# Performance work log

Measured on AMD Instinct MI355X. Metric: run time of the kernel, lower is better.

Reference implementation:

```python
import jax, jax.numpy as jnp
import numpy as np

S, B, I, H, L = 512, 64, 128, 256, 6  # seq_len, batch, input, hidden, layers


def setup_inputs() -> dict:
    key = jax.random.key(0)
    ks = jax.random.split(key, 8)
    sc = 1.0 / np.sqrt(H)
    return {
        "x": jax.random.normal(ks[0], (S, B, I), jnp.float32),
        "h0": jax.random.normal(ks[1], (2 * L, B, H), jnp.float32),
        "w_ih0": jax.random.normal(ks[2], (2, 3 * H, I), jnp.float32) * sc,
        "b_ih0": jax.random.normal(ks[3], (2, 3 * H), jnp.float32) * sc,
        "w_ih": jax.random.normal(ks[4], (L - 1, 2, 3 * H, 2 * H), jnp.float32) * sc,
        "b_ih": jax.random.normal(ks[5], (L - 1, 2, 3 * H), jnp.float32) * sc,
        "w_hh": jax.random.normal(ks[6], (L, 2, 3 * H, H), jnp.float32) * sc,
        "b_hh": jax.random.normal(ks[7], (L, 2, 3 * H), jnp.float32) * sc,
    }


def _gru_direction(gi_seq, h0d, whh, bhh, reverse):
    # gi_seq: (S, B, 3H) precomputed input gates; h0d: (B, H)
    if reverse:
        gi_seq = gi_seq[::-1]

    def step(h, gi):
        gh = h @ whh.T + bhh                       # (B, 3H)
        gi_r, gi_z, gi_n = jnp.split(gi, 3, axis=-1)
        gh_r, gh_z, gh_n = jnp.split(gh, 3, axis=-1)
        r = jax.nn.sigmoid(gi_r + gh_r)
        z = jax.nn.sigmoid(gi_z + gh_z)
        n = jnp.tanh(gi_n + r * gh_n)
        h_new = (1.0 - z) * n + z * h
        return h_new, h_new

    h_n, outs = jax.lax.scan(step, h0d, gi_seq)
    if reverse:
        outs = outs[::-1]
    return h_n, outs  # (B,H), (S,B,H)


def reference(x, h0, w_ih0, b_ih0, w_ih, b_ih, w_hh, b_hh):
    cur = x
    finals = []
    for l in range(L):
        wi = w_ih0 if l == 0 else w_ih[l - 1]
        bi = b_ih0 if l == 0 else b_ih[l - 1]
        # precompute input-gate projections for the whole sequence (big GEMM)
        gi_f = jnp.einsum('sbi,gi->sbg', cur, wi[0]) + bi[0]
        gi_b = jnp.einsum('sbi,gi->sbg', cur, wi[1]) + bi[1]
        h_f, out_f = _gru_direction(gi_f, h0[2 * l], w_hh[l, 0], b_hh[l, 0], False)
        h_b, out_b = _gru_direction(gi_b, h0[2 * l + 1], w_hh[l, 1], b_hh[l, 1], True)
        finals.append(h_f)
        finals.append(h_b)
        if l < L - 1:
            cur = jnp.concatenate([out_f, out_b], axis=-1)  # (S, B, 2H)
    return jnp.stack(finals)  # (2L, B, H)
```

## Files before the change

### kernel.cpp

```cpp
#include <hip/hip_runtime.h>
#include <hip/hip_bf16.h>
#include <cstddef>

#define S_LEN 512
#define BATCH 64
#define HID 256
#define G3 768
#define SB (S_LEN*BATCH)
#define D2 512
#define L2E 1.44269504f

typedef unsigned short u16;
typedef _Float16 h2v __attribute__((ext_vector_type(2)));
typedef __attribute__((ext_vector_type(8))) short s16x8;
typedef __attribute__((ext_vector_type(4))) float f32x4;

__device__ __forceinline__ float bf2f(u16 u) {
    return __uint_as_float(((unsigned)u) << 16);
}
__device__ __forceinline__ u16 f2bf(float f) {
    unsigned u = __float_as_uint(f);
    unsigned r = (u + 0x7FFFu + ((u >> 16) & 1u)) >> 16;
    return (u16)r;
}
__device__ __forceinline__ u16 f2h_bits(float f) {
    _Float16 h = (_Float16)f;
    union { _Float16 h; u16 u; } cv; cv.h = h;
    return cv.u;
}
__device__ __forceinline__ h2v u2h(unsigned u) {
    union { unsigned u; h2v h; } cv; cv.u = u;
    return cv.h;
}
__device__ __forceinline__ float dot2f(unsigned w, unsigned h, float acc) {
#if __has_builtin(__builtin_amdgcn_fdot2)
    return __builtin_amdgcn_fdot2(u2h(w), u2h(h), acc, false);
#else
    h2v wv = u2h(w), hv = u2h(h);
    return acc + (float)wv.x * (float)hv.x + (float)wv.y * (float)hv.y;
#endif
}
__device__ __forceinline__ float fast_rcp(float x) {
#if __has_builtin(__builtin_amdgcn_rcpf)
    return __builtin_amdgcn_rcpf(x);
#else
    return 1.f / x;
#endif
}
__device__ __forceinline__ float fast_exp2(float x) {
#if __has_builtin(__builtin_amdgcn_exp2f)
    return __builtin_amdgcn_exp2f(x);
#else
    return __expf(x * 0.69314718f);
#endif
}
__device__ __forceinline__ void gload_lds16(const void* g, void* l) {
    __builtin_amdgcn_global_load_lds((const __attribute__((address_space(1))) void*)g,
                                     (__attribute__((address_space(3))) void*)l, 16, 0, 0);
}

__global__ void f32_to_bf16(const float* __restrict__ in, u16* __restrict__ out, long n) {
    long i = (long)blockIdx.x * 256 + threadIdx.x;
    if (i < n) out[i] = f2bf(in[i]);
}
__global__ void f32_to_bf16_gs(const float* __restrict__ in, u16* __restrict__ out,
                               long n, int K) {
    long i = (long)blockIdx.x * 256 + threadIdx.x;
    if (i >= n) return;
    int g = (int)((i / K) % 768);
    float sc = (g < 512) ? L2E : (2.f * L2E);
    out[i] = f2bf(in[i] * sc);
}
__global__ void pack_whh_f16_gs(const float* __restrict__ in, unsigned* __restrict__ out,
                                long total) {
    long i = (long)blockIdx.x * 256 + threadIdx.x;
    if (i >= total) return;
    long mat = i / (128L * G3);
    long rem = i - mat * (128L * G3);
    int k2 = (int)(rem / G3);
    int g  = (int)(rem - (long)k2 * G3);
    float sc = (g < 512) ? L2E : (2.f * L2E);
    const float* base = in + mat * (768L * 256) + (long)g * 256 + 2 * k2;
    unsigned lo = f2h_bits(base[0] * sc);
    unsigned hi = f2h_bits(base[1] * sc);
    out[i] = lo | (hi << 16);
}
__global__ void add_bias(const float* __restrict__ bih0, const float* __restrict__ bihl,
                         const float* __restrict__ bhh, float* __restrict__ outb) {
    int i = blockIdx.x * 256 + threadIdx.x;
    if (i >= 6 * 1536) return;
    int l = i / 1536, r = i - l * 1536;
    int g = r % 768;
    float bi = (l == 0) ? bih0[r] : bihl[(l - 1) * 1536 + r];
    outb[i] = (g < 512) ? (bi + bhh[i]) * L2E : bi * (2.f * L2E);
}

__global__ __launch_bounds__(256, 2) void gemm_mfma(
    const u16* __restrict__ A,
    const u16* __restrict__ Bt,
    const float* __restrict__ bias,
    u16* __restrict__ Cg,
    int K)
{
    int d = blockIdx.z;
    const u16* Bb = Bt + (size_t)d * 768 * K;
    const float* bi = bias + d * G3;
    u16* Cm = Cg + (size_t)d * SB * G3;

    int n0 = blockIdx.x * 128;
    int m0 = blockIdx.y * 128;
    int tid = threadIdx.x;
    int wave = tid >> 6, lane = tid & 63;
    int wm = wave >> 1, wn = wave & 1;

    __shared__ u16 Asm[128 * 32];
    __shared__ u16 Bsm[128 * 32];

    f32x4 acc[4][4] = {};

    for (int k0 = 0; k0 < K; k0 += 32) {
#pragma unroll
        for (int p = 0; p < 2; p++) {
            int c = p * 256 + wave * 64 + lane;
            int row = c >> 2, kc = c & 3;
            const u16* srcA = A + (size_t)(m0 + row) * K + k0 + kc * 8;
            const u16* srcB = Bb + (size_t)(n0 + row) * K + k0 + kc * 8;
            gload_lds16(srcA, &Asm[(p * 256 + wave * 64) * 8]);
            gload_lds16(srcB, &Bsm[(p * 256 + wave * 64) * 8]);
        }
        __syncthreads();

        s16x8 af[4], bfr[4];
#pragma unroll
        for (int i = 0; i < 4; i++) {
            int arow = wm * 64 + i * 16 + (lane & 15);
            af[i] = *reinterpret_cast<const s16x8*>(&Asm[arow * 32 + (lane >> 4) * 8]);
            int brow = wn * 64 + i * 16 + (lane & 15);
            bfr[i] = *reinterpret_cast<const s16x8*>(&Bsm[brow * 32 + (lane >> 4) * 8]);
        }
#pragma unroll
        for (int i = 0; i < 4; i++)
#pragma unroll
            for (int j = 0; j < 4; j++)
                acc[i][j] = __builtin_amdgcn_mfma_f32_16x16x32_bf16(af[i], bfr[j], acc[i][j], 0, 0, 0);
        __syncthreads();
    }

    int lcol = lane & 15, lrow4 = (lane >> 4) * 4;
#pragma unroll
    for (int i = 0; i < 4; i++) {
#pragma unroll
        for (int j = 0; j < 4; j++) {
            int n = n0 + wn * 64 + j * 16 + lcol;
            float bv = bi[n];
#pragma unroll
            for (int q = 0; q < 4; q++) {
                int m = m0 + wm * 64 + i * 16 + lrow4 + q;
                Cm[(size_t)m * G3 + n] = f2bf(acc[i][j][q] + bv);
            }
        }
    }
}

__global__ __launch_bounds__(768, 3) void gru_scan(
    const unsigned* __restrict__ wpack,
    const float* __restrict__ bhh,
    const u16* __restrict__ gi,
    const float* __restrict__ h0,
    u16* __restrict__ outc,
    float* __restrict__ finals,
    int layer)
{
    int b = blockIdx.x;
    int d = blockIdx.y;
    int tid = threadIdx.x;

    int ld = layer * 2 + d;
    const unsigned* Wp = wpack + (size_t)ld * 128 * G3 + tid;
    const u16* gid = gi + (size_t)d * SB * G3;

    __shared__ float rz_s[512];
    __shared__ alignas(16) _Float16 h16_s[HID];
    __shared__ u16 gi_s[2][G3];

    unsigned wpk[128];
#pragma unroll
    for (int k = 0; k < 128; k++) wpk[k] = Wp[(size_t)k * G3];

    int gate = tid >> 8;
    int j = tid & 255;

    float hreg = 0.f, bhn = 0.f;
    if (gate == 2) {
        hreg = h0[(size_t)ld * BATCH * HID + b * HID + j];
        bhn = bhh[(size_t)ld * G3 + 512 + j] * (2.f * L2E);
        h16_s[j] = (_Float16)hreg;
    }
    {
        int s0 = d ? (S_LEN - 1) : 0;
        gi_s[0][tid] = gid[((size_t)s0 * BATCH + b) * G3 + tid];
    }
    __syncthreads();

    for (int t = 0; t < S_LEN; t++) {
        int s = d ? (S_LEN - 1 - t) : t;
        u16 ginext = 0;
        if (t + 1 < S_LEN) {
            int sn = d ? (s - 1) : (s + 1);
            ginext = gid[((size_t)sn * BATCH + b) * G3 + tid];
        }
        float acc = 0.f;
        const uint4* hp = reinterpret_cast<const uint4*>(h16_s);
#pragma unroll
        for (int k = 0; k < 32; k++) {
            uint4 q = hp[k];
            acc = dot2f(wpk[4 * k + 0], q.x, acc);
            acc = dot2f(wpk[4 * k + 1], q.y, acc);
            acc = dot2f(wpk[4 * k + 2], q.z, acc);
            acc = dot2f(wpk[4 * k + 3], q.w, acc);
        }
        float giv = bf2f(gi_s[t & 1][tid]);
        gi_s[(t + 1) & 1][tid] = ginext;
        if (gate < 2)
            rz_s[tid] = fast_rcp(1.f + fast_exp2(-(giv + acc)));
        __syncthreads();
        if (gate == 2) {
            float r = rz_s[j];
            float z = rz_s[256 + j];
            float xn2 = giv + r * (acc + bhn);
            float n = 1.f - 2.f * fast_rcp(fast_exp2(xn2) + 1.f);
            float hn = n + z * (hreg - n);
            hreg = hn;
            h16_s[j] = (_Float16)hn;
            outc[((size_t)s * BATCH + b) * D2 + d * HID + j] = f2bf(hn);
        }
        __syncthreads();
    }
    if (gate == 2)
        finals[(size_t)ld * BATCH * HID + b * HID + j] = hreg;
}

extern "C" void kernel_launch(void* const* d_in, const int* in_sizes, int n_in,
                              void* d_out, int out_size, void* d_ws, size_t ws_size,
                              hipStream_t stream) {
    const float* x     = (const float*)d_in[0];
    const float* h0    = (const float*)d_in[1];
    const float* w_ih0 = (const float*)d_in[2];
    const float* b_ih0 = (const float*)d_in[3];
    const float* w_ih  = (const float*)d_in[4];
    const float* b_ih  = (const float*)d_in[5];
    const float* w_hh  = (const float*)d_in[6];
    const float* b_hh  = (const float*)d_in[7];
    float* out = (float*)d_out;

    char* ws = (char*)d_ws;
    unsigned* wpack = (unsigned*)(ws + 0);
    u16* wbf0  = (u16*)(ws + 4718592);
    u16* wbfl  = (u16*)(ws + 5111808);
    float* biasT = (float*)(ws + 12976128);
    u16* gi    = (u16*)(ws + 13012992);
    u16* curA  = (u16*)(ws + 113676288);
    u16* curB  = (u16*)(ws + 147230720);

    pack_whh_f16_gs<<<(1179648 + 255) / 256, 256, 0, stream>>>(w_hh, wpack, 1179648L);
    f32_to_bf16_gs<<<(196608 + 255) / 256, 256, 0, stream>>>(w_ih0, wbf0, 196608L, 128);
    f32_to_bf16_gs<<<(3932160 + 255) / 256, 256, 0, stream>>>(w_ih, wbfl, 3932160L, 512);
    f32_to_bf16<<<(4194304 + 255) / 256, 256, 0, stream>>>(x, curA, 4194304L);
    add_bias<<<(9216 + 255) / 256, 256, 0, stream>>>(b_ih0, b_ih, b_hh, biasT);

    u16* cin = curA;
    u16* cout_ = curB;
    for (int l = 0; l < 6; l++) {
        int K = l ? 512 : 128;
        const u16* wt = l ? (wbfl + (size_t)(l - 1) * 2 * 768 * 512) : wbf0;
        const float* bi = biasT + (size_t)l * 1536;
        dim3 g(6, 256, 2);
        gemm_mfma<<<g, 256, 0, stream>>>(cin, wt, bi, gi, K);
        gru_scan<<<dim3(64, 2), 768, 0, stream>>>(wpack, b_hh, gi, h0,
                                                  cout_, out, l);
        u16* tmp = cin; cin = cout_; cout_ = tmp;
    }
}
```

Before: 3.913 ms.

## Split hidden dot across lane pairs to halve LDS reads in GRU scan

Repacks W_hh so each adjacent lane pair splits the k dimension: each lane reads only half of the hidden state from LDS and computes partial sums for both gates of the pair, then exchanges one partial with its neighbour via a shuffle. It also uses four independent accumulators to break the serial dot2 dependency chain. This aims to cut LDS bandwidth and latency in the recurrent step, at the cost of a cross-lane shuffle and a more complex weight layout.

```diff
diff --git a/kernel.cpp b/kernel.cpp
--- a/kernel.cpp
+++ b/kernel.cpp
@@ -71,16 +71,20 @@
     float sc = (g < 512) ? L2E : (2.f * L2E);
     out[i] = f2bf(in[i] * sc);
 }
-__global__ void pack_whh_f16_gs(const float* __restrict__ in, unsigned* __restrict__ out,
-                                long total) {
+__global__ void pack_whh_pair(const float* __restrict__ in, unsigned* __restrict__ out,
+                              long total) {
     long i = (long)blockIdx.x * 256 + threadIdx.x;
     if (i >= total) return;
     long mat = i / (128L * G3);
     long rem = i - mat * (128L * G3);
-    int k2 = (int)(rem / G3);
-    int g  = (int)(rem - (long)k2 * G3);
-    float sc = (g < 512) ? L2E : (2.f * L2E);
-    const float* base = in + mat * (768L * 256) + (long)g * 256 + 2 * k2;
+    int j = (int)(rem / G3);
+    int lane = (int)(rem - (long)j * G3);
+    int p = lane & 1;
+    int g0 = lane & ~1;
+    int gate = (j < 64) ? g0 : (g0 + 1);
+    int kp = 64 * p + ((j < 64) ? j : (j - 64));
+    float sc = (gate < 512) ? L2E : (2.f * L2E);
+    const float* base = in + mat * (768L * 256) + (long)gate * 256 + 2 * kp;
     unsigned lo = f2h_bits(base[0] * sc);
     unsigned hi = f2h_bits(base[1] * sc);
     out[i] = lo | (hi << 16);
@@ -163,7 +167,7 @@
 }
 
 __global__ __launch_bounds__(768, 3) void gru_scan(
-    const unsigned* __restrict__ wpack,
+    const unsigned* __restrict__ wpack2,
     const float* __restrict__ bhh,
     const u16* __restrict__ gi,
     const float* __restrict__ h0,
@@ -176,7 +180,7 @@
     int tid = threadIdx.x;
 
     int ld = layer * 2 + d;
-    const unsigned* Wp = wpack + (size_t)ld * 128 * G3 + tid;
+    const unsigned* Wp = wpack2 + (size_t)ld * 128 * G3 + tid;
     const u16* gid = gi + (size_t)d * SB * G3;
 
     __shared__ float rz_s[512];
@@ -189,6 +193,7 @@
 
     int gate = tid >> 8;
     int j = tid & 255;
+    int p = tid & 1;
 
     float hreg = 0.f, bhn = 0.f;
     if (gate == 2) {
@@ -209,16 +214,36 @@
             int sn = d ? (s - 1) : (s + 1);
             ginext = gid[((size_t)sn * BATCH + b) * G3 + tid];
         }
-        float acc = 0.f;
-        const uint4* hp = reinterpret_cast<const uint4*>(h16_s);
-#pragma unroll
-        for (int k = 0; k < 32; k++) {
-            uint4 q = hp[k];
-            acc = dot2f(wpk[4 * k + 0], q.x, acc);
-            acc = dot2f(wpk[4 * k + 1], q.y, acc);
-            acc = dot2f(wpk[4 * k + 2], q.z, acc);
-            acc = dot2f(wpk[4 * k + 3], q.w, acc);
-        }
+        const uint4* hp = reinterpret_cast<const uint4*>(h16_s) + p * 16;
+        float a0 = 0.f, a1 = 0.f, b0v = 0.f, b1v = 0.f;
+#pragma unroll
+        for (int u = 0; u < 16; u += 2) {
+            uint4 q0 = hp[u];
+            uint4 q1 = hp[u + 1];
+            a0 = dot2f(wpk[4 * u + 0], q0.x, a0);
+            a0 = dot2f(wpk[4 * u + 1], q0.y, a0);
+            a0 = dot2f(wpk[4 * u + 2], q0.z, a0);
+            a0 = dot2f(wpk[4 * u + 3], q0.w, a0);
+            a1 = dot2f(wpk[4 * u + 4], q1.x, a1);
+            a1 = dot2f(wpk[4 * u + 5], q1.y, a1);
+            a1 = dot2f(wpk[4 * u + 6], q1.z, a1);
+            a1 = dot2f(wpk[4 * u + 7], q1.w, a1);
+            b0v = dot2f(wpk[64 + 4 * u + 0], q0.x, b0v);
+            b0v = dot2f(wpk[64 + 4 * u + 1], q0.y, b0v);
+            b0v = dot2f(wpk[64 + 4 * u + 2], q0.z, b0v);
+            b0v = dot2f(wpk[64 + 4 * u + 3], q0.w, b0v);
+            b1v = dot2f(wpk[64 + 4 * u + 4], q1.x, b1v);
+            b1v = dot2f(wpk[64 + 4 * u + 5], q1.y, b1v);
+            b1v = dot2f(wpk[64 + 4 * u + 6], q1.z, b1v);
+            b1v = dot2f(wpk[64 + 4 * u + 7], q1.w, b1v);
+        }
+        float pg0 = a0 + a1;
+        float pg1 = b0v + b1v;
+        float own   = p ? pg1 : pg0;
+        float other = p ? pg0 : pg1;
+        float recv = __shfl_xor(other, 1, 64);
+        float acc = own + recv;
+
         float giv = bf2f(gi_s[t & 1][tid]);
         gi_s[(t + 1) & 1][tid] = ginext;
         if (gate < 2)
@@ -254,7 +279,7 @@
     float* out = (float*)d_out;
 
     char* ws = (char*)d_ws;
-    unsigned* wpack = (unsigned*)(ws + 0);
+    unsigned* wpack2 = (unsigned*)(ws + 0);
     u16* wbf0  = (u16*)(ws + 4718592);
     u16* wbfl  = (u16*)(ws + 5111808);
     float* biasT = (float*)(ws + 12976128);
@@ -262,7 +287,7 @@
     u16* curA  = (u16*)(ws + 113676288);
     u16* curB  = (u16*)(ws + 147230720);
 
-    pack_whh_f16_gs<<<(1179648 + 255) / 256, 256, 0, stream>>>(w_hh, wpack, 1179648L);
+    pack_whh_pair<<<(1179648 + 255) / 256, 256, 0, stream>>>(w_hh, wpack2, 1179648L);
     f32_to_bf16_gs<<<(196608 + 255) / 256, 256, 0, stream>>>(w_ih0, wbf0, 196608L, 128);
     f32_to_bf16_gs<<<(3932160 + 255) / 256, 256, 0, stream>>>(w_ih, wbfl, 3932160L, 512);
     f32_to_bf16<<<(4194304 + 255) / 256, 256, 0, stream>>>(x, curA, 4194304L);
@@ -276,7 +301,7 @@
         const float* bi = biasT + (size_t)l * 1536;
         dim3 g(6, 256, 2);
         gemm_mfma<<<g, 256, 0, stream>>>(cin, wt, bi, gi, K);
-        gru_scan<<<dim3(64, 2), 768, 0, stream>>>(wpack, b_hh, gi, h0,
+        gru_scan<<<dim3(64, 2), 768, 0, stream>>>(wpack2, b_hh, gi, h0,
                                                   cout_, out, l);
         u16* tmp = cin; cin = cout_; cout_ = tmp;
     }
```

Result: slower. 4.066 ms (+3.9%).

## Restructure GRU scan to quad-split hidden units with one barrier per step

Applied to the files above, without the earlier changes.

The recurrent scan now gives each hidden unit to four threads. Each of the four holds a quarter of the K dimension for all three gates, and the partial sums are reduced with lane shuffles. This removes the r/z shared-memory exchange and one of the two block barriers per timestep. The h buffer is double-buffered, with swizzled LDS reads to avoid bank conflicts, and the input-gate prefetch now runs two steps ahead. The block grows to 1024 threads with 96 weight registers each, and the pack kernel is rewritten for the new layout, which raises register-pressure and occupancy risk.

```diff
diff --git a/kernel.cpp b/kernel.cpp
--- a/kernel.cpp
+++ b/kernel.cpp
@@ -71,16 +71,21 @@
     float sc = (g < 512) ? L2E : (2.f * L2E);
     out[i] = f2bf(in[i] * sc);
 }
-__global__ void pack_whh_f16_gs(const float* __restrict__ in, unsigned* __restrict__ out,
-                                long total) {
+__global__ void pack_whh_quad(const float* __restrict__ in, unsigned* __restrict__ out,
+                              long total) {
     long i = (long)blockIdx.x * 256 + threadIdx.x;
     if (i >= total) return;
-    long mat = i / (128L * G3);
-    long rem = i - mat * (128L * G3);
-    int k2 = (int)(rem / G3);
-    int g  = (int)(rem - (long)k2 * G3);
-    float sc = (g < 512) ? L2E : (2.f * L2E);
-    const float* base = in + mat * (768L * 256) + (long)g * 256 + 2 * k2;
+    long mat = i / (96L * 1024);
+    long rem = i - mat * (96L * 1024);
+    int j = (int)(rem / 1024);
+    int tid = (int)(rem - (long)j * 1024);
+    int unit = tid >> 2, p = tid & 3;
+    int gsel = j / 32, jj = j % 32, ii = jj / 4, m = jj % 4;
+    int c = (ii + 2 * p) & 7;
+    int k = 64 * p + 8 * c + 2 * m;
+    int gate = gsel * 256 + unit;
+    float sc = (gate < 512) ? L2E : (2.f * L2E);
+    const float* base = in + mat * (768L * 256) + (long)gate * 256 + k;
     unsigned lo = f2h_bits(base[0] * sc);
     unsigned hi = f2h_bits(base[1] * sc);
     out[i] = lo | (hi << 16);
@@ -162,8 +167,8 @@
     }
 }
 
-__global__ __launch_bounds__(768, 3) void gru_scan(
-    const unsigned* __restrict__ wpack,
+__global__ __launch_bounds__(1024, 4) void gru_scan(
+    const unsigned* __restrict__ wpack4,
     const float* __restrict__ bhh,
     const u16* __restrict__ gi,
     const float* __restrict__ h0,
@@ -174,70 +179,80 @@
     int b = blockIdx.x;
     int d = blockIdx.y;
     int tid = threadIdx.x;
+    int unit = tid >> 2;
+    int p = tid & 3;
 
     int ld = layer * 2 + d;
-    const unsigned* Wp = wpack + (size_t)ld * 128 * G3 + tid;
+    const unsigned* Wp = wpack4 + (size_t)ld * 96 * 1024 + tid;
     const u16* gid = gi + (size_t)d * SB * G3;
 
-    __shared__ float rz_s[512];
-    __shared__ alignas(16) _Float16 h16_s[HID];
+    __shared__ alignas(16) _Float16 hbuf[2][HID];
     __shared__ u16 gi_s[2][G3];
 
-    unsigned wpk[128];
-#pragma unroll
-    for (int k = 0; k < 128; k++) wpk[k] = Wp[(size_t)k * G3];
-
-    int gate = tid >> 8;
-    int j = tid & 255;
-
-    float hreg = 0.f, bhn = 0.f;
-    if (gate == 2) {
-        hreg = h0[(size_t)ld * BATCH * HID + b * HID + j];
-        bhn = bhh[(size_t)ld * G3 + 512 + j] * (2.f * L2E);
-        h16_s[j] = (_Float16)hreg;
-    }
+    unsigned wpk[96];
+#pragma unroll
+    for (int j = 0; j < 96; j++) wpk[j] = Wp[(size_t)j * 1024];
+
+    float hreg = h0[(size_t)ld * BATCH * HID + b * HID + unit];
+    float bhn = bhh[(size_t)ld * G3 + 512 + unit] * (2.f * L2E);
+    if (p == 0) hbuf[0][unit] = (_Float16)hreg;
+
+    u16 greg = 0;
     {
         int s0 = d ? (S_LEN - 1) : 0;
-        gi_s[0][tid] = gid[((size_t)s0 * BATCH + b) * G3 + tid];
+        if (tid < G3) gi_s[0][tid] = gid[((size_t)s0 * BATCH + b) * G3 + tid];
+        int s1 = d ? (S_LEN - 2) : 1;
+        if (tid < G3) greg = gid[((size_t)s1 * BATCH + b) * G3 + tid];
     }
     __syncthreads();
 
     for (int t = 0; t < S_LEN; t++) {
         int s = d ? (S_LEN - 1 - t) : t;
-        u16 ginext = 0;
-        if (t + 1 < S_LEN) {
-            int sn = d ? (s - 1) : (s + 1);
-            ginext = gid[((size_t)sn * BATCH + b) * G3 + tid];
-        }
-        float acc = 0.f;
-        const uint4* hp = reinterpret_cast<const uint4*>(h16_s);
-#pragma unroll
-        for (int k = 0; k < 32; k++) {
-            uint4 q = hp[k];
-            acc = dot2f(wpk[4 * k + 0], q.x, acc);
-            acc = dot2f(wpk[4 * k + 1], q.y, acc);
-            acc = dot2f(wpk[4 * k + 2], q.z, acc);
-            acc = dot2f(wpk[4 * k + 3], q.w, acc);
-        }
-        float giv = bf2f(gi_s[t & 1][tid]);
-        gi_s[(t + 1) & 1][tid] = ginext;
-        if (gate < 2)
-            rz_s[tid] = fast_rcp(1.f + fast_exp2(-(giv + acc)));
-        __syncthreads();
-        if (gate == 2) {
-            float r = rz_s[j];
-            float z = rz_s[256 + j];
-            float xn2 = giv + r * (acc + bhn);
-            float n = 1.f - 2.f * fast_rcp(fast_exp2(xn2) + 1.f);
-            float hn = n + z * (hreg - n);
-            hreg = hn;
-            h16_s[j] = (_Float16)hn;
-            outc[((size_t)s * BATCH + b) * D2 + d * HID + j] = f2bf(hn);
-        }
-        __syncthreads();
-    }
-    if (gate == 2)
-        finals[(size_t)ld * BATCH * HID + b * HID + j] = hreg;
+        int par = t & 1;
+        if (t + 1 < S_LEN && tid < G3) gi_s[par ^ 1][tid] = greg;
+        if (t + 2 < S_LEN && tid < G3) {
+            int s2 = d ? (s - 2) : (s + 2);
+            greg = gid[((size_t)s2 * BATCH + b) * G3 + tid];
+        }
+        const char* hb = (const char*)&hbuf[par][0] + p * 128;
+        float a0 = 0.f, a1 = 0.f, a2 = 0.f;
+#pragma unroll
+        for (int ii = 0; ii < 8; ii++) {
+            uint4 q = *(const uint4*)(hb + (((ii + 2 * p) & 7) << 4));
+            int jb = 4 * ii;
+            a0 = dot2f(wpk[jb + 0], q.x, a0);
+            a0 = dot2f(wpk[jb + 1], q.y, a0);
+            a0 = dot2f(wpk[jb + 2], q.z, a0);
+            a0 = dot2f(wpk[jb + 3], q.w, a0);
+            a1 = dot2f(wpk[32 + jb + 0], q.x, a1);
+            a1 = dot2f(wpk[32 + jb + 1], q.y, a1);
+            a1 = dot2f(wpk[32 + jb + 2], q.z, a1);
+            a1 = dot2f(wpk[32 + jb + 3], q.w, a1);
+            a2 = dot2f(wpk[64 + jb + 0], q.x, a2);
+            a2 = dot2f(wpk[64 + jb + 1], q.y, a2);
+            a2 = dot2f(wpk[64 + jb + 2], q.z, a2);
+            a2 = dot2f(wpk[64 + jb + 3], q.w, a2);
+        }
+        a0 += __shfl_xor(a0, 1, 64); a0 += __shfl_xor(a0, 2, 64);
+        a1 += __shfl_xor(a1, 1, 64); a1 += __shfl_xor(a1, 2, 64);
+        a2 += __shfl_xor(a2, 1, 64); a2 += __shfl_xor(a2, 2, 64);
+        float gir = bf2f(gi_s[par][unit]);
+        float giz = bf2f(gi_s[par][256 + unit]);
+        float gin = bf2f(gi_s[par][512 + unit]);
+        float r = fast_rcp(1.f + fast_exp2(-(gir + a0)));
+        float z = fast_rcp(1.f + fast_exp2(-(giz + a1)));
+        float xn2 = gin + r * (a2 + bhn);
+        float n = 1.f - 2.f * fast_rcp(fast_exp2(xn2) + 1.f);
+        float hn = n + z * (hreg - n);
+        hreg = hn;
+        if (p == 0) hbuf[par ^ 1][unit] = (_Float16)hn;
+        if (p == 1) outc[((size_t)s * BATCH + b) * D2 + d * HID + unit] = f2bf(hn);
+        asm volatile("s_waitcnt lgkmcnt(0)" ::: "memory");
+        __builtin_amdgcn_s_barrier();
+        __builtin_amdgcn_sched_barrier(0);
+    }
+    if (p == 0)
+        finals[(size_t)ld * BATCH * HID + b * HID + unit] = hreg;
 }
 
 extern "C" void kernel_launch(void* const* d_in, const int* in_sizes, int n_in,
@@ -254,7 +269,7 @@
     float* out = (float*)d_out;
 
     char* ws = (char*)d_ws;
-    unsigned* wpack = (unsigned*)(ws + 0);
+    unsigned* wpack4 = (unsigned*)(ws + 0);
     u16* wbf0  = (u16*)(ws + 4718592);
     u16* wbfl  = (u16*)(ws + 5111808);
     float* biasT = (float*)(ws + 12976128);
@@ -262,7 +277,7 @@
     u16* curA  = (u16*)(ws + 113676288);
     u16* curB  = (u16*)(ws + 147230720);
 
-    pack_whh_f16_gs<<<(1179648 + 255) / 256, 256, 0, stream>>>(w_hh, wpack, 1179648L);
+    pack_whh_quad<<<(1179648 + 255) / 256, 256, 0, stream>>>(w_hh, wpack4, 1179648L);
     f32_to_bf16_gs<<<(196608 + 255) / 256, 256, 0, stream>>>(w_ih0, wbf0, 196608L, 128);
     f32_to_bf16_gs<<<(3932160 + 255) / 256, 256, 0, stream>>>(w_ih, wbfl, 3932160L, 512);
     f32_to_bf16<<<(4194304 + 255) / 256, 256, 0, stream>>>(x, curA, 4194304L);
@@ -276,8 +291,8 @@
         const float* bi = biasT + (size_t)l * 1536;
         dim3 g(6, 256, 2);
         gemm_mfma<<<g, 256, 0, stream>>>(cin, wt, bi, gi, K);
-        gru_scan<<<dim3(64, 2), 768, 0, stream>>>(wpack, b_hh, gi, h0,
-                                                  cout_, out, l);
+        gru_scan<<<dim3(64, 2), 1024, 0, stream>>>(wpack4, b_hh, gi, h0,
+                                                   cout_, out, l);
         u16* tmp = cin; cin = cout_; cout_ = tmp;
     }
 }
```

Result: slower. 4.736 ms (+21.0%).
